# Kernel tuning notes

Hardware: AMD Instinct MI355X
Metric: run time of the kernel (lower is better)

Reference implementation:

```python
import jax, jax.numpy as jnp
import numpy as np

WS = (2, 7, 7)      # window size
SS = (1, 3, 3)      # shift size
NH = 8              # num heads
DIM = 256
N = WS[0] * WS[1] * WS[2]   # 98 tokens per window
EPS = 1e-5


def _ln(x, w, b):
    m = jnp.mean(x, -1, keepdims=True)
    v = jnp.mean((x - m) ** 2, -1, keepdims=True)
    return (x - m) / jnp.sqrt(v + EPS) * w + b


def _rel_index():
    coords = np.stack(np.meshgrid(np.arange(WS[0]), np.arange(WS[1]), np.arange(WS[2]), indexing='ij'))
    cf = coords.reshape(3, -1)
    rc = (cf[:, :, None] - cf[:, None, :]).transpose(1, 2, 0).astype(np.int64)
    rc[..., 0] += WS[0] - 1
    rc[..., 1] += WS[1] - 1
    rc[..., 2] += WS[2] - 1
    rc[..., 0] *= (2 * WS[1] - 1) * (2 * WS[2] - 1)
    rc[..., 1] *= 2 * WS[2] - 1
    return rc.sum(-1).astype(np.int32)  # [N, N]


def _attn_mask(Dp, Hp, Wp):
    img = np.zeros((1, Dp, Hp, Wp, 1), np.float32)
    cnt = 0
    def sl(ws, ss):
        return (slice(0, -ws), slice(-ws, -ss), slice(-ss, None))
    for d in sl(WS[0], SS[0]):
        for h in sl(WS[1], SS[1]):
            for w in sl(WS[2], SS[2]):
                img[:, d, h, w, :] = cnt
                cnt += 1
    mw = img.reshape(1, Dp // WS[0], WS[0], Hp // WS[1], WS[1], Wp // WS[2], WS[2], 1)
    mw = mw.transpose(0, 1, 3, 5, 2, 4, 6, 7).reshape(-1, N)
    am = mw[:, None, :] - mw[:, :, None]
    return np.where(am != 0, np.float32(-100.0), np.float32(0.0)).astype(np.float32)  # [nW, N, N]


def setup_inputs() -> dict:
    key = jax.random.key(0)
    ks = jax.random.split(key, 6)
    B, D, H, W, C = 2, 16, 56, 56, DIM
    hid = 4 * C
    return {
        'x': jax.random.normal(ks[0], (B, D, H, W, C), jnp.float32),
        'mask_matrix': jnp.asarray(_attn_mask(D, H, W)),
        'rel_index': jnp.asarray(_rel_index()),
        'rel_bias_table': 0.02 * jax.random.normal(ks[1], ((2 * WS[0] - 1) * (2 * WS[1] - 1) * (2 * WS[2] - 1), NH), jnp.float32),
        'norm1_w': jnp.ones((C,), jnp.float32), 'norm1_b': jnp.zeros((C,), jnp.float32),
        'qkv_w': 0.02 * jax.random.normal(ks[2], (3 * C, C), jnp.float32), 'qkv_b': jnp.zeros((3 * C,), jnp.float32),
        'proj_w': 0.02 * jax.random.normal(ks[3], (C, C), jnp.float32), 'proj_b': jnp.zeros((C,), jnp.float32),
        'norm2_w': jnp.ones((C,), jnp.float32), 'norm2_b': jnp.zeros((C,), jnp.float32),
        'fc1_w': 0.02 * jax.random.normal(ks[4], (hid, C), jnp.float32), 'fc1_b': jnp.zeros((hid,), jnp.float32),
        'fc2_w': 0.02 * jax.random.normal(ks[5], (C, hid), jnp.float32), 'fc2_b': jnp.zeros((C,), jnp.float32),
    }


def _forward(x, mask_matrix, rel_index, rel_bias_table, norm1_w, norm1_b, qkv_w, qkv_b,
             proj_w, proj_b, norm2_w, norm2_b, fc1_w, fc1_b, fc2_w, fc2_b):
    B, D, H, W, C = x.shape
    nh, hd = NH, C // NH
    scale = hd ** -0.5
    nd, nhw, nww = D // WS[0], H // WS[1], W // WS[2]

    # --- part 1: norm -> shift -> window attention -> unshift ---
    h = _ln(x, norm1_w, norm1_b)
    h = jnp.roll(h, (-SS[0], -SS[1], -SS[2]), axis=(1, 2, 3))
    # window partition -> [B_, N, C]
    h = h.reshape(B, nd, WS[0], nhw, WS[1], nww, WS[2], C)
    h = h.transpose(0, 1, 3, 5, 2, 4, 6, 7).reshape(-1, N, C)
    B_ = h.shape[0]

    qkv = (h @ qkv_w.T + qkv_b).reshape(B_, N, 3, nh, hd).transpose(2, 0, 3, 1, 4)
    q, k, v = qkv[0], qkv[1], qkv[2]   # [B_, nh, N, hd]
    attn = jnp.einsum('bhnd,bhmd->bhnm', q * scale, k)
    bias = rel_bias_table[rel_index.reshape(-1)].reshape(N, N, nh).transpose(2, 0, 1)
    attn = attn + bias[None]
    nW = mask_matrix.shape[0]
    attn = attn.reshape(B_ // nW, nW, nh, N, N) + mask_matrix[None, :, None]
    attn = jax.nn.softmax(attn.reshape(B_, nh, N, N), axis=-1)
    o = jnp.einsum('bhnm,bhmd->bhnd', attn, v).transpose(0, 2, 1, 3).reshape(B_, N, C)
    o = o @ proj_w.T + proj_b
    # window reverse -> [B, D, H, W, C]
    o = o.reshape(B, nd, nhw, nww, WS[0], WS[1], WS[2], C)
    o = o.transpose(0, 1, 4, 2, 5, 3, 6, 7).reshape(B, D, H, W, C)
    o = jnp.roll(o, SS, axis=(1, 2, 3))

    x = x + o
    # --- part 2: MLP ---
    h2 = _ln(x, norm2_w, norm2_b)
    h2 = jax.nn.gelu(h2 @ fc1_w.T + fc1_b, approximate=False)
    return x + (h2 @ fc2_w.T + fc2_b)


def reference(x, mask_matrix, rel_index, rel_bias_table, norm1_w, norm1_b, qkv_w, qkv_b,
              proj_w, proj_b, norm2_w, norm2_b, fc1_w, fc1_b, fc2_w, fc2_b):
    return _forward(x, mask_matrix, rel_index, rel_bias_table, norm1_w, norm1_b, qkv_w, qkv_b,
                    proj_w, proj_b, norm2_w, norm2_b, fc1_w, fc1_b, fc2_w, fc2_b)
```

## Files before the change

kernel.cpp:

```cpp
#include <hip/hip_runtime.h>
#include <hip/hip_bf16.h>

typedef __attribute__((ext_vector_type(8))) short bf16x8;
typedef __attribute__((ext_vector_type(4))) float f32x4;

__device__ __forceinline__ unsigned short f2bf(float f){
  __hip_bfloat16 h = __float2bfloat16(f);
  return *reinterpret_cast<unsigned short*>(&h);
}

#define GLDS16(gptr, lptr) \
  __builtin_amdgcn_global_load_lds((const __attribute__((address_space(1))) unsigned int*)(gptr), \
                                   (__attribute__((address_space(3))) unsigned int*)(lptr), 16, 0, 0)

__global__ void cvtk(const float* __restrict__ s, unsigned short* __restrict__ d, int n){
  int i = blockIdx.x*256 + threadIdx.x;
  if (i < n) d[i] = f2bf(s[i]);
}

__global__ void combok(const int* __restrict__ ri, const float* __restrict__ tbl,
                       const float* __restrict__ mask, unsigned short* __restrict__ out){
  int g = blockIdx.x*256 + threadIdx.x;
  if (g >= 802816) return;
  int r = g & 3;
  int t = g >> 2;
  int lane = t & 63; t >>= 6;
  int nt = t % 7; t /= 7;
  int mt = t % 7; t /= 7;
  int p = t >> 3, h = t & 7;
  int gi = mt*16 + (lane >> 4)*4 + r; if (gi > 97) gi = 97;
  int j  = nt*16 + (lane & 15);
  float v;
  if (j < 98){
    int wrep = ((p&4)?448:0) + ((p&2)?56:0) + ((p&1)?7:0);
    v = tbl[ri[gi*98 + j]*8 + h] + mask[(size_t)wrep*9604 + gi*98 + j];
  } else {
    v = -30000.f;
  }
  out[g] = f2bf(v);
}

__launch_bounds__(256)
__global__ void lnk(const float* __restrict__ xin, const float* __restrict__ gw, const float* __restrict__ gb,
                    unsigned short* __restrict__ hout, int mode)
{
  int wid = threadIdx.x >> 6, lane = threadIdx.x & 63;
  int tok = blockIdx.x*4 + wid;
  int src;
  if (mode == 0){
    int w = tok / 98, n = tok % 98;
    int b = w >> 9, rr = w & 511;
    int di = rr >> 6, hi = (rr >> 3) & 7, wi = rr & 7;
    int d2 = n / 49, n2 = n % 49, h2 = n2 / 7, w2 = n2 % 7;
    int sd = (di*2 + d2 + 1) & 15;
    int sh = hi*7 + h2 + 3; if (sh >= 56) sh -= 56;
    int sw = wi*7 + w2 + 3; if (sw >= 56) sw -= 56;
    src = ((b*16 + sd)*56 + sh)*56 + sw;
  } else {
    src = tok;
  }
  float4 v = *(const float4*)(xin + (size_t)src*256 + lane*4);
  float s  = v.x + v.y + v.z + v.w;
  float s2 = v.x*v.x + v.y*v.y + v.z*v.z + v.w*v.w;
  #pragma unroll
  for (int off = 1; off < 64; off <<= 1){
    s  += __shfl_xor(s, off);
    s2 += __shfl_xor(s2, off);
  }
  float mean = s * (1.f/256.f);
  float var  = s2 * (1.f/256.f) - mean*mean;
  float rstd = rsqrtf(var + 1e-5f);
  int c = lane*4;
  float4 wv = *(const float4*)(gw + c);
  float4 bv = *(const float4*)(gb + c);
  unsigned int p0 = (unsigned int)f2bf((v.x-mean)*rstd*wv.x + bv.x)
                  | ((unsigned int)f2bf((v.y-mean)*rstd*wv.y + bv.y) << 16);
  unsigned int p1 = (unsigned int)f2bf((v.z-mean)*rstd*wv.z + bv.z)
                  | ((unsigned int)f2bf((v.w-mean)*rstd*wv.w + bv.w) << 16);
  uint2 pk; pk.x = p0; pk.y = p1;
  *(uint2*)(hout + (size_t)tok*256 + c) = pk;
}

template<int EPI>
__launch_bounds__(256, 2)
__global__ void gemmk(const unsigned short* __restrict__ A, const unsigned short* __restrict__ Bw,
                      const float* __restrict__ bias, int K, int nbx,
                      unsigned short* __restrict__ outb, const float* __restrict__ xres,
                      float* __restrict__ outf, int moff)
{
  __shared__ unsigned short As[128*32];
  __shared__ unsigned short Bs[128*32];
  int tid = threadIdx.x;
  int wid = tid >> 6, lane = tid & 63, l16 = lane & 15, lk = lane >> 4;
  int wm = wid >> 1, wn = wid & 1;
  int cpx = gridDim.x >> 3;
  int swb = (blockIdx.x & 7)*cpx + (blockIdx.x >> 3);
  int mblk = swb / nbx, nblk = swb % nbx;
  const unsigned short* Ab = A  + (size_t)mblk*128*K;
  const unsigned short* Bb = Bw + (size_t)nblk*128*K;
  int rA = tid >> 2;
  int kcA = (((tid & 3) ^ ((tid >> 3) & 3)))*8;
  int sx = (l16 >> 1) & 3;

  f32x4 acc[4][4];
  #pragma unroll
  for (int i = 0; i < 4; i++)
    #pragma unroll
    for (int j = 0; j < 4; j++)
      acc[i][j] = (f32x4){0.f,0.f,0.f,0.f};

  for (int ks = 0; ks < K; ks += 32){
    __syncthreads();
    GLDS16(Ab + (size_t)rA*K      + ks + kcA, &As[wid*512]);
    GLDS16(Ab + (size_t)(rA+64)*K + ks + kcA, &As[2048 + wid*512]);
    GLDS16(Bb + (size_t)rA*K      + ks + kcA, &Bs[wid*512]);
    GLDS16(Bb + (size_t)(rA+64)*K + ks + kcA, &Bs[2048 + wid*512]);
    __syncthreads();
    bf16x8 af[4], bfr[4];
    #pragma unroll
    for (int mi = 0; mi < 4; mi++) af[mi]  = *(const bf16x8*)&As[(wm*64 + mi*16 + l16)*32 + (lk ^ sx)*8];
    #pragma unroll
    for (int ni = 0; ni < 4; ni++) bfr[ni] = *(const bf16x8*)&Bs[(wn*64 + ni*16 + l16)*32 + (lk ^ sx)*8];
    #pragma unroll
    for (int mi = 0; mi < 4; mi++)
      #pragma unroll
      for (int ni = 0; ni < 4; ni++)
        acc[mi][ni] = __builtin_amdgcn_mfma_f32_16x16x32_bf16(af[mi], bfr[ni], acc[mi][ni], 0, 0, 0);
  }

  int rowb = mblk*128 + wm*64;
  int colb = nblk*128 + wn*64;
  #pragma unroll
  for (int mi = 0; mi < 4; mi++){
    #pragma unroll
    for (int r = 0; r < 4; r++){
      int row = rowb + mi*16 + lk*4 + r;
      if constexpr (EPI == 0){
        #pragma unroll
        for (int ni = 0; ni < 4; ni++){
          int col = colb + ni*16 + l16;
          float v = acc[mi][ni][r] + bias[col];
          if (col < 256) v *= 0.17677669529663687f;
          outb[(size_t)row*768 + col] = f2bf(v);
        }
      } else if constexpr (EPI == 1){
        int w = row / 98, n = row % 98;
        int b = w >> 9, rr = w & 511;
        int di = rr >> 6, hi = (rr >> 3) & 7, wi = rr & 7;
        int d2 = n / 49, n2 = n % 49, h2 = n2 / 7, w2 = n2 % 7;
        int sd = (di*2 + d2 + 1) & 15;
        int sh = hi*7 + h2 + 3; if (sh >= 56) sh -= 56;
        int sw = wi*7 + w2 + 3; if (sw >= 56) sw -= 56;
        size_t tnat = (((size_t)b*16 + sd)*56 + sh)*56 + sw;
        #pragma unroll
        for (int ni = 0; ni < 4; ni++){
          int col = colb + ni*16 + l16;
          float v = acc[mi][ni][r] + bias[col];
          outf[tnat*256 + col] = xres[tnat*256 + col] + v;
        }
      } else if constexpr (EPI == 2){
        #pragma unroll
        for (int ni = 0; ni < 4; ni++){
          int col = colb + ni*16 + l16;
          float v = acc[mi][ni][r] + bias[col];
          float gl = v * 0.5f * (1.f + erff(v * 0.70710678118654752f));
          outb[(size_t)row*1024 + col] = f2bf(gl);
        }
      } else {
        #pragma unroll
        for (int ni = 0; ni < 4; ni++){
          int col = colb + ni*16 + l16;
          float v = acc[mi][ni][r] + bias[col];
          outf[((size_t)(moff + row))*256 + col] += v;
        }
      }
    }
  }
}

__launch_bounds__(256)
__global__ void attnk(const unsigned short* __restrict__ qkv, const unsigned short* __restrict__ comboX,
                      unsigned short* __restrict__ obuf)
{
  __shared__ unsigned short P[4][16*136];
  int tid = threadIdx.x, wid = tid >> 6, lane = tid & 63, l16 = lane & 15, lk = lane >> 4;
  int cpx = gridDim.x >> 3;
  int swb = (blockIdx.x & 7)*cpx + (blockIdx.x >> 3);
  int task = swb*4 + wid;
  int w = task >> 3, h = task & 7;
  int rr = w & 511;
  int pat = (((rr>>6)==7)?4:0) | ((((rr>>3)&7)==7)?2:0) | (((rr&7)==7)?1:0);
  const unsigned short* cb = comboX + (size_t)(pat*8 + h)*12544;
  const unsigned short* base = qkv + (size_t)w*98*768 + h*32;

  bf16x8 v0[4], v1[4];
  #pragma unroll
  for (int kcc = 0; kcc < 4; kcc++){
    #pragma unroll
    for (int j = 0; j < 8; j++){
      int k = kcc*32 + lk*8 + j; if (k > 97) k = 97;
      unsigned int u = *(const unsigned int*)(base + (size_t)k*768 + 512 + 2*l16);
      v0[kcc][j] = (short)(u & 0xffff);
      v1[kcc][j] = (short)(u >> 16);
    }
  }

  unsigned short* Pw = &P[wid][0];
  { int rp = lane >> 2, cc = 112 + (lane & 3)*4;
    *(uint2*)&Pw[rp*136 + cc] = make_uint2(0u, 0u); }

  for (int mt = 0; mt < 7; mt++){
    int qrow = mt*16 + l16; if (qrow > 97) qrow = 97;
    bf16x8 qa = *(const bf16x8*)(base + (size_t)qrow*768 + lk*8);

    const unsigned short* cm = cb + mt*1792;
    f32x4 s[7];
    #pragma unroll
    for (int nt = 0; nt < 7; nt++){
      int kc = nt*16 + l16; if (kc > 97) kc = 97;
      bf16x8 kf = *(const bf16x8*)(base + (size_t)kc*768 + 256 + lk*8);
      uint2 c2 = *(const uint2*)(cm + (nt*64 + lane)*4);
      f32x4 ci;
      ci[0] = __uint_as_float(c2.x << 16);
      ci[1] = __uint_as_float(c2.x & 0xffff0000u);
      ci[2] = __uint_as_float(c2.y << 16);
      ci[3] = __uint_as_float(c2.y & 0xffff0000u);
      s[nt] = __builtin_amdgcn_mfma_f32_16x16x32_bf16(qa, kf, ci, 0, 0, 0);
    }

    float mx[4] = {-3e38f,-3e38f,-3e38f,-3e38f};
    #pragma unroll
    for (int nt = 0; nt < 7; nt++){
      mx[0] = fmaxf(mx[0], s[nt][0]); mx[1] = fmaxf(mx[1], s[nt][1]);
      mx[2] = fmaxf(mx[2], s[nt][2]); mx[3] = fmaxf(mx[3], s[nt][3]);
    }
    #pragma unroll
    for (int r = 0; r < 4; r++){
      #pragma unroll
      for (int off = 1; off < 16; off <<= 1) mx[r] = fmaxf(mx[r], __shfl_xor(mx[r], off));
    }
    float sm[4] = {0.f,0.f,0.f,0.f};
    #pragma unroll
    for (int r = 0; r < 4; r++){
      #pragma unroll
      for (int nt = 0; nt < 7; nt++){
        float e = __expf(s[nt][r] - mx[r]);
        s[nt][r] = e; sm[r] += e;
      }
    }
    #pragma unroll
    for (int r = 0; r < 4; r++){
      #pragma unroll
      for (int off = 1; off < 16; off <<= 1) sm[r] += __shfl_xor(sm[r], off);
      sm[r] = 1.f / sm[r];
    }

    #pragma unroll
    for (int r = 0; r < 4; r++)
      #pragma unroll
      for (int nt = 0; nt < 7; nt++)
        Pw[(lk*4 + r)*136 + nt*16 + l16] = f2bf(s[nt][r]*sm[r]);

    f32x4 o0 = (f32x4){0.f,0.f,0.f,0.f}, o1 = (f32x4){0.f,0.f,0.f,0.f};
    #pragma unroll
    for (int kcc = 0; kcc < 4; kcc++){
      bf16x8 pa = *(const bf16x8*)&Pw[l16*136 + kcc*32 + lk*8];
      __builtin_amdgcn_s_setprio(1);
      o0 = __builtin_amdgcn_mfma_f32_16x16x32_bf16(pa, v0[kcc], o0, 0, 0, 0);
      o1 = __builtin_amdgcn_mfma_f32_16x16x32_bf16(pa, v1[kcc], o1, 0, 0, 0);
      __builtin_amdgcn_s_setprio(0);
    }
    #pragma unroll
    for (int r = 0; r < 4; r++){
      int n = mt*16 + lk*4 + r;
      if (n < 98){
        unsigned int pk = (unsigned int)f2bf(o0[r]) | ((unsigned int)f2bf(o1[r]) << 16);
        *(unsigned int*)(obuf + ((size_t)w*98 + n)*256 + h*32 + 2*l16) = pk;
      }
    }
  }
}

extern "C" void kernel_launch(void* const* d_in, const int* in_sizes, int n_in,
                              void* d_out, int out_size, void* d_ws, size_t ws_size,
                              hipStream_t stream)
{
  const float* x     = (const float*)d_in[0];
  const float* maskm = (const float*)d_in[1];
  const int*   ri    = (const int*)d_in[2];
  const float* tbl   = (const float*)d_in[3];
  const float* n1w   = (const float*)d_in[4];
  const float* n1b   = (const float*)d_in[5];
  const float* qkvw  = (const float*)d_in[6];
  const float* qkvbv = (const float*)d_in[7];
  const float* projw = (const float*)d_in[8];
  const float* projb = (const float*)d_in[9];
  const float* n2w   = (const float*)d_in[10];
  const float* n2b   = (const float*)d_in[11];
  const float* fc1w  = (const float*)d_in[12];
  const float* fc1b  = (const float*)d_in[13];
  const float* fc2w  = (const float*)d_in[14];
  const float* fc2b  = (const float*)d_in[15];
  float* dout = (float*)d_out;
  char* ws = (char*)d_ws;

  unsigned short* qkvB  = (unsigned short*)(ws + 0);
  unsigned short* hb    = (unsigned short*)(ws + 154140672);
  unsigned short* wq    = (unsigned short*)(ws + 205520896);
  unsigned short* comboX= (unsigned short*)(ws + 205914112);
  unsigned short* wp    = (unsigned short*)(ws + 0);
  unsigned short* h2 = (unsigned short*)(ws + 0);
  unsigned short* g  = (unsigned short*)(ws + 51380224);
  unsigned short* w1 = (unsigned short*)(ws + 154140672);
  unsigned short* w2 = (unsigned short*)(ws + 154664960);

  cvtk<<<768, 256, 0, stream>>>(qkvw, wq, 196608);
  combok<<<3136, 256, 0, stream>>>(ri, tbl, maskm, comboX);

  lnk<<<25088, 256, 0, stream>>>(x, n1w, n1b, hb, 0);
  gemmk<0><<<784*6, 256, 0, stream>>>(hb, wq, qkvbv, 256, 6, qkvB, nullptr, nullptr, 0);
  attnk<<<2048, 256, 0, stream>>>(qkvB, comboX, hb);
  cvtk<<<256, 256, 0, stream>>>(projw, wp, 65536);
  gemmk<1><<<784*2, 256, 0, stream>>>(hb, wp, projb, 256, 2, nullptr, x, dout, 0);

  cvtk<<<1024, 256, 0, stream>>>(fc1w, w1, 262144);
  cvtk<<<1024, 256, 0, stream>>>(fc2w, w2, 262144);
  lnk<<<25088, 256, 0, stream>>>(dout, n2w, n2b, h2, 1);
  for (int c = 0; c < 2; c++){
    gemmk<2><<<392*8, 256, 0, stream>>>(h2 + (size_t)c*50176*256, w1, fc1b, 256, 8, g, nullptr, nullptr, 0);
    gemmk<3><<<392*2, 256, 0, stream>>>(g, w2, fc2b, 1024, 2, nullptr, nullptr, dout, c*50176);
  }
}
```

Measured before the change: 487.3 us.

## Double-buffer GEMM LDS tiles and streamline window-attention softmax

The GEMM kernel now double-buffers its A/B LDS tiles. It issues the next k-slice's global-to-LDS loads before computing on the current one, leaving one barrier per iteration, and raises the occupancy hint to 4 blocks per CU. The attention kernel hoists the K fragments out of the query-tile loop. It replaces the per-row max reduction with one wave-wide max per 16-row tile, and computes row sums with an extra MFMA against a ones vector, normalising at output. This cuts shuffles and exps and overlaps memory with MFMA. The cost is more LDS and register pressure, plus possible precision loss if rows in a tile have very different maxima.

```diff
diff --git a/kernel.cpp b/kernel.cpp
--- a/kernel.cpp
+++ b/kernel.cpp
@@ -82,14 +82,14 @@
 }
 
 template<int EPI>
-__launch_bounds__(256, 2)
+__launch_bounds__(256, 4)
 __global__ void gemmk(const unsigned short* __restrict__ A, const unsigned short* __restrict__ Bw,
                       const float* __restrict__ bias, int K, int nbx,
                       unsigned short* __restrict__ outb, const float* __restrict__ xres,
                       float* __restrict__ outf, int moff)
 {
-  __shared__ unsigned short As[128*32];
-  __shared__ unsigned short Bs[128*32];
+  __shared__ unsigned short As[2][4096];
+  __shared__ unsigned short Bs[2][4096];
   int tid = threadIdx.x;
   int wid = tid >> 6, lane = tid & 63, l16 = lane & 15, lk = lane >> 4;
   int wm = wid >> 1, wn = wid & 1;
@@ -102,6 +102,13 @@
   int kcA = (((tid & 3) ^ ((tid >> 3) & 3)))*8;
   int sx = (l16 >> 1) & 3;
 
+#define STAGE(bufi, kss) do { \
+    GLDS16(Ab + (size_t)rA*K      + (kss) + kcA, &As[bufi][wid*512]); \
+    GLDS16(Ab + (size_t)(rA+64)*K + (kss) + kcA, &As[bufi][2048 + wid*512]); \
+    GLDS16(Bb + (size_t)rA*K      + (kss) + kcA, &Bs[bufi][wid*512]); \
+    GLDS16(Bb + (size_t)(rA+64)*K + (kss) + kcA, &Bs[bufi][2048 + wid*512]); \
+  } while(0)
+
   f32x4 acc[4][4];
   #pragma unroll
   for (int i = 0; i < 4; i++)
@@ -109,24 +116,25 @@
     for (int j = 0; j < 4; j++)
       acc[i][j] = (f32x4){0.f,0.f,0.f,0.f};
 
+  STAGE(0, 0);
+  __syncthreads();
+  int cur = 0;
   for (int ks = 0; ks < K; ks += 32){
-    __syncthreads();
-    GLDS16(Ab + (size_t)rA*K      + ks + kcA, &As[wid*512]);
-    GLDS16(Ab + (size_t)(rA+64)*K + ks + kcA, &As[2048 + wid*512]);
-    GLDS16(Bb + (size_t)rA*K      + ks + kcA, &Bs[wid*512]);
-    GLDS16(Bb + (size_t)(rA+64)*K + ks + kcA, &Bs[2048 + wid*512]);
-    __syncthreads();
+    if (ks + 32 < K) STAGE(cur ^ 1, ks + 32);
     bf16x8 af[4], bfr[4];
     #pragma unroll
-    for (int mi = 0; mi < 4; mi++) af[mi]  = *(const bf16x8*)&As[(wm*64 + mi*16 + l16)*32 + (lk ^ sx)*8];
-    #pragma unroll
-    for (int ni = 0; ni < 4; ni++) bfr[ni] = *(const bf16x8*)&Bs[(wn*64 + ni*16 + l16)*32 + (lk ^ sx)*8];
+    for (int mi = 0; mi < 4; mi++) af[mi]  = *(const bf16x8*)&As[cur][(wm*64 + mi*16 + l16)*32 + (lk ^ sx)*8];
+    #pragma unroll
+    for (int ni = 0; ni < 4; ni++) bfr[ni] = *(const bf16x8*)&Bs[cur][(wn*64 + ni*16 + l16)*32 + (lk ^ sx)*8];
     #pragma unroll
     for (int mi = 0; mi < 4; mi++)
       #pragma unroll
       for (int ni = 0; ni < 4; ni++)
         acc[mi][ni] = __builtin_amdgcn_mfma_f32_16x16x32_bf16(af[mi], bfr[ni], acc[mi][ni], 0, 0, 0);
-  }
+    __syncthreads();
+    cur ^= 1;
+  }
+#undef STAGE
 
   int rowb = mblk*128 + wm*64;
   int colb = nblk*128 + wn*64;
@@ -193,6 +201,12 @@
   const unsigned short* cb = comboX + (size_t)(pat*8 + h)*12544;
   const unsigned short* base = qkv + (size_t)w*98*768 + h*32;
 
+  bf16x8 kfr[7];
+  #pragma unroll
+  for (int nt = 0; nt < 7; nt++){
+    int kc = nt*16 + l16; if (kc > 97) kc = 97;
+    kfr[nt] = *(const bf16x8*)(base + (size_t)kc*768 + 256 + lk*8);
+  }
   bf16x8 v0[4], v1[4];
   #pragma unroll
   for (int kcc = 0; kcc < 4; kcc++){
@@ -204,6 +218,9 @@
       v1[kcc][j] = (short)(u >> 16);
     }
   }
+  bf16x8 vones;
+  #pragma unroll
+  for (int j = 0; j < 8; j++) vones[j] = (short)0x3F80;
 
   unsigned short* Pw = &P[wid][0];
   { int rp = lane >> 2, cc = 112 + (lane & 3)*4;
@@ -217,15 +234,13 @@
     f32x4 s[7];
     #pragma unroll
     for (int nt = 0; nt < 7; nt++){
-      int kc = nt*16 + l16; if (kc > 97) kc = 97;
-      bf16x8 kf = *(const bf16x8*)(base + (size_t)kc*768 + 256 + lk*8);
       uint2 c2 = *(const uint2*)(cm + (nt*64 + lane)*4);
       f32x4 ci;
       ci[0] = __uint_as_float(c2.x << 16);
       ci[1] = __uint_as_float(c2.x & 0xffff0000u);
       ci[2] = __uint_as_float(c2.y << 16);
       ci[3] = __uint_as_float(c2.y & 0xffff0000u);
-      s[nt] = __builtin_amdgcn_mfma_f32_16x16x32_bf16(qa, kf, ci, 0, 0, 0);
+      s[nt] = __builtin_amdgcn_mfma_f32_16x16x32_bf16(qa, kfr[nt], ci, 0, 0, 0);
     }
 
     float mx[4] = {-3e38f,-3e38f,-3e38f,-3e38f};
@@ -234,47 +249,33 @@
       mx[0] = fmaxf(mx[0], s[nt][0]); mx[1] = fmaxf(mx[1], s[nt][1]);
       mx[2] = fmaxf(mx[2], s[nt][2]); mx[3] = fmaxf(mx[3], s[nt][3]);
     }
-    #pragma unroll
-    for (int r = 0; r < 4; r++){
-      #pragma unroll
-      for (int off = 1; off < 16; off <<= 1) mx[r] = fmaxf(mx[r], __shfl_xor(mx[r], off));
-    }
-    float sm[4] = {0.f,0.f,0.f,0.f};
-    #pragma unroll
-    for (int r = 0; r < 4; r++){
-      #pragma unroll
-      for (int nt = 0; nt < 7; nt++){
-        float e = __expf(s[nt][r] - mx[r]);
-        s[nt][r] = e; sm[r] += e;
-      }
-    }
-    #pragma unroll
-    for (int r = 0; r < 4; r++){
-      #pragma unroll
-      for (int off = 1; off < 16; off <<= 1) sm[r] += __shfl_xor(sm[r], off);
-      sm[r] = 1.f / sm[r];
-    }
+    float mxa = fmaxf(fmaxf(mx[0], mx[1]), fmaxf(mx[2], mx[3]));
+    #pragma unroll
+    for (int off = 1; off < 64; off <<= 1) mxa = fmaxf(mxa, __shfl_xor(mxa, off));
 
     #pragma unroll
     for (int r = 0; r < 4; r++)
       #pragma unroll
       for (int nt = 0; nt < 7; nt++)
-        Pw[(lk*4 + r)*136 + nt*16 + l16] = f2bf(s[nt][r]*sm[r]);
+        Pw[(lk*4 + r)*136 + nt*16 + l16] = f2bf(__expf(s[nt][r] - mxa));
 
     f32x4 o0 = (f32x4){0.f,0.f,0.f,0.f}, o1 = (f32x4){0.f,0.f,0.f,0.f};
+    f32x4 os = (f32x4){0.f,0.f,0.f,0.f};
     #pragma unroll
     for (int kcc = 0; kcc < 4; kcc++){
       bf16x8 pa = *(const bf16x8*)&Pw[l16*136 + kcc*32 + lk*8];
       __builtin_amdgcn_s_setprio(1);
       o0 = __builtin_amdgcn_mfma_f32_16x16x32_bf16(pa, v0[kcc], o0, 0, 0, 0);
       o1 = __builtin_amdgcn_mfma_f32_16x16x32_bf16(pa, v1[kcc], o1, 0, 0, 0);
+      os = __builtin_amdgcn_mfma_f32_16x16x32_bf16(pa, vones,   os, 0, 0, 0);
       __builtin_amdgcn_s_setprio(0);
     }
     #pragma unroll
     for (int r = 0; r < 4; r++){
       int n = mt*16 + lk*4 + r;
       if (n < 98){
-        unsigned int pk = (unsigned int)f2bf(o0[r]) | ((unsigned int)f2bf(o1[r]) << 16);
+        float inv = __builtin_amdgcn_rcpf(os[r]);
+        unsigned int pk = (unsigned int)f2bf(o0[r]*inv) | ((unsigned int)f2bf(o1[r]*inv) << 16);
         *(unsigned int*)(obuf + ((size_t)w*98 + n)*256 + h*32 + 2*l16) = pk;
       }
     }
```

Result: no change. 485.7 us (-0.3%).
